# Performance work log

Measured on AMD Instinct MI355X. Metric: run time of the kernel, lower is better.

Reference implementation:

```python
import jax, jax.numpy as jnp
import numpy as np

B, D, N, F = 2048, 512, 100000, 64
NEG = -1000000.0


def setup_inputs() -> dict:
    key = jax.random.key(0)
    k1, k2, k3, k4 = jax.random.split(key, 4)
    q = jax.random.normal(k1, (B, D), dtype=jnp.float32)
    rhs = jax.random.normal(k2, (D, N), dtype=jnp.float32)
    queries = jax.random.randint(k3, (B, 3), 0, N, dtype=jnp.int64)
    filter_idx = jax.random.randint(k4, (B, F), 0, N, dtype=jnp.int64)
    return {"q": q, "rhs": rhs, "queries": queries, "filter_idx": filter_idx}


def reference(q, rhs, queries, filter_idx):
    # targets[i] = score of the true triple = q[i] . rhs[:, true_rhs[i]]
    true_rhs = queries[:, 2]                         # [B]
    targets = jnp.einsum('bd,bd->b', q, rhs[:, true_rhs].T)  # [B]

    scores = q @ rhs                                  # [B, N]

    # filtered ranking: mask out known true tails + the query's own tail
    rows = jnp.arange(scores.shape[0])[:, None]       # [B, 1]
    scores = scores.at[rows, filter_idx].set(NEG)
    scores = scores.at[jnp.arange(scores.shape[0]), true_rhs].set(NEG)

    # rank = 1 + number of candidates scoring >= the true triple
    ranks = 1.0 + jnp.sum((scores >= targets[:, None]).astype(jnp.float32), axis=1)
    return ranks
```

## Files before the change

kernel.cpp:

```cpp
#include <hip/hip_runtime.h>
#include <hip/hip_bf16.h>

#define B_ 2048
#define D_ 512
#define N_ 100000
#define F_ 64
#define NEGV (-1000000.0f)

typedef __bf16 bfx8 __attribute__((ext_vector_type(8)));
typedef float f32x4 __attribute__((ext_vector_type(4)));
typedef unsigned short u16x8 __attribute__((ext_vector_type(8)));

static __device__ __forceinline__ unsigned short f2bf(float f) {
  unsigned u = __float_as_uint(f);
  unsigned r = (u + 0x7fffu + ((u >> 16) & 1u)) >> 16;
  return (unsigned short)r;
}
static __device__ __forceinline__ float bf2f(unsigned short u) {
  return __uint_as_float(((unsigned)u) << 16);
}

static __device__ __forceinline__ void async_copy16(const void* g, void* l) {
  __builtin_amdgcn_global_load_lds((const __attribute__((address_space(1))) void*)g,
                                   (__attribute__((address_space(3))) void*)l, 16, 0, 0);
}

__global__ void targets_init(const float* __restrict__ q, const float* __restrict__ rhs,
                             const int* __restrict__ queries, float* __restrict__ targets,
                             float* __restrict__ out) {
  __shared__ float wsum[4];
  int b = blockIdx.x;
  int tid = threadIdx.x, lane = tid & 63, w = tid >> 6;
  int p = queries[b * 3 + 2];
  float s = 0.f;
  for (int d = tid; d < D_; d += 256) s += q[b * D_ + d] * rhs[(size_t)d * N_ + p];
  for (int off = 32; off; off >>= 1) s += __shfl_down(s, off, 64);
  if (lane == 0) wsum[w] = s;
  __syncthreads();
  if (tid == 0) {
    targets[b] = wsum[0] + wsum[1] + wsum[2] + wsum[3];
    out[b] = 1.0f;
  }
}

__global__ void convert_q(const float* __restrict__ q, unsigned short* __restrict__ qb) {
  int i = blockIdx.x * blockDim.x + threadIdx.x;
  const float4* q4 = (const float4*)q;
  float4 v = q4[i];
  ushort4 o;
  o.x = f2bf(v.x); o.y = f2bf(v.y); o.z = f2bf(v.z); o.w = f2bf(v.w);
  ((ushort4*)qb)[i] = o;
}

__global__ void transpose_rhs(const float* __restrict__ rhs, unsigned short* __restrict__ rt) {
  __shared__ float tile[64][65];
  int n0 = blockIdx.x * 64, d0 = blockIdx.y * 64;
  int tid = threadIdx.x;
  if (n0 + 64 <= N_) {
#pragma unroll
    for (int p = 0; p < 4; ++p) {
      int e = p * 256 + tid;
      int d = e >> 4, c4 = e & 15;
      float4 v = *(const float4*)(rhs + (size_t)(d0 + d) * N_ + n0 + c4 * 4);
      tile[d][c4 * 4 + 0] = v.x; tile[d][c4 * 4 + 1] = v.y;
      tile[d][c4 * 4 + 2] = v.z; tile[d][c4 * 4 + 3] = v.w;
    }
  } else {
    int c = tid & 63, r4 = tid >> 6;
#pragma unroll
    for (int p = 0; p < 16; ++p) {
      int d = r4 + p * 4;
      if (n0 + c < N_) tile[d][c] = rhs[(size_t)(d0 + d) * N_ + n0 + c];
    }
  }
  __syncthreads();
#pragma unroll
  for (int p = 0; p < 4; ++p) {
    int e = p * 256 + tid;
    int n = e >> 4, dg = e & 15;
    if (n0 + n < N_) {
      ushort4 o;
      o.x = f2bf(tile[dg * 4 + 0][n]);
      o.y = f2bf(tile[dg * 4 + 1][n]);
      o.z = f2bf(tile[dg * 4 + 2][n]);
      o.w = f2bf(tile[dg * 4 + 3][n]);
      *(ushort4*)(rt + (size_t)(n0 + n) * D_ + d0 + dg * 4) = o;
    }
  }
}

__global__ void __launch_bounds__(256) gemm_count(
    const unsigned short* __restrict__ qb,
    const unsigned short* __restrict__ rt,
    const float* __restrict__ targets,
    float* __restrict__ out) {
  __shared__ unsigned short As[128 * 64];
  __shared__ unsigned short Bs[128 * 64];
  __shared__ float sT[128];
  __shared__ int cnt2[2][128];

  int tid = threadIdx.x;
  int m0 = blockIdx.x * 128;
  int n0 = blockIdx.y * 128;

  if (tid < 128) sT[tid] = targets[m0 + tid];

  int w = tid >> 6, lane = tid & 63;
  int mw = (w & 1) * 64, nw = (w >> 1) * 64;
  int quad = lane >> 4, l16 = lane & 15;

  f32x4 acc[4][4];
  f32x4 z = {0.f, 0.f, 0.f, 0.f};
#pragma unroll
  for (int i = 0; i < 4; ++i)
#pragma unroll
    for (int j = 0; j < 4; ++j) acc[i][j] = z;

  for (int kt = 0; kt < 8; ++kt) {
    int k0 = kt * 64;
    __syncthreads();
#pragma unroll
    for (int i = 0; i < 4; ++i) {
      int c = i * 256 + tid;
      int m = c >> 3, jj = c & 7;
      const unsigned short* gp = qb + (size_t)(m0 + m) * D_ + k0 + jj * 8;
      async_copy16(gp, As + c * 8);
    }
#pragma unroll
    for (int i = 0; i < 4; ++i) {
      int c = i * 256 + tid;
      int n = c >> 3, jj = c & 7;
      int ng = n0 + n; if (ng > N_ - 1) ng = N_ - 1;
      const unsigned short* gp = rt + (size_t)ng * D_ + k0 + jj * 8;
      async_copy16(gp, Bs + c * 8);
    }
    __syncthreads();

#pragma unroll
    for (int kh = 0; kh < 2; ++kh) {
      bfx8 a[4], b[4];
#pragma unroll
      for (int mi = 0; mi < 4; ++mi) {
        int m = mw + mi * 16 + l16;
        u16x8 au = *(const u16x8*)(As + m * 64 + kh * 32 + quad * 8);
        a[mi] = __builtin_bit_cast(bfx8, au);
      }
#pragma unroll
      for (int ni = 0; ni < 4; ++ni) {
        int n = nw + ni * 16 + l16;
        u16x8 bu = *(const u16x8*)(Bs + n * 64 + kh * 32 + quad * 8);
        b[ni] = __builtin_bit_cast(bfx8, bu);
      }
#pragma unroll
      for (int mi = 0; mi < 4; ++mi)
#pragma unroll
        for (int ni = 0; ni < 4; ++ni)
          acc[mi][ni] = __builtin_amdgcn_mfma_f32_16x16x32_bf16(a[mi], b[ni], acc[mi][ni], 0, 0, 0);
    }
  }

#pragma unroll
  for (int mi = 0; mi < 4; ++mi) {
#pragma unroll
    for (int reg = 0; reg < 4; ++reg) {
      int rl = mw + mi * 16 + quad * 4 + reg;
      float t = sT[rl];
      int c = 0;
#pragma unroll
      for (int ni = 0; ni < 4; ++ni) {
        int col = n0 + nw + ni * 16 + l16;
        if (col < N_ && acc[mi][ni][reg] >= t) c++;
      }
      c += __shfl_xor(c, 1, 64);
      c += __shfl_xor(c, 2, 64);
      c += __shfl_xor(c, 4, 64);
      c += __shfl_xor(c, 8, 64);
      if (l16 == 0) cnt2[w >> 1][rl] = c;
    }
  }
  __syncthreads();
  if (tid < 128) {
    int tot = cnt2[0][tid] + cnt2[1][tid];
    if (tot) atomicAdd(&out[m0 + tid], (float)tot);
  }
}

__global__ void corrections(const unsigned short* __restrict__ qb,
                            const unsigned short* __restrict__ rt,
                            const int* __restrict__ queries,
                            const int* __restrict__ filt,
                            const float* __restrict__ targets,
                            float* __restrict__ out) {
  int b = blockIdx.x;
  int tid = threadIdx.x;
  int w = tid >> 6, lane = tid & 63;
  __shared__ int idx[F_ + 1];
  __shared__ unsigned char uq[F_ + 1];
  if (tid <= F_) idx[tid] = (tid < F_) ? filt[b * F_ + tid] : queries[b * 3 + 2];
  __syncthreads();
  if (tid <= F_) {
    int p = idx[tid];
    bool u = true;
    for (int j = 0; j < tid; ++j)
      if (idx[j] == p) u = false;
    uq[tid] = u;
  }
  __syncthreads();
  float t = targets[b];
  float corr = 0.f;
  u16x8 qv = ((const u16x8*)(qb + (size_t)b * D_))[lane];
  for (int ii = w; ii <= F_; ii += 8) {
    if (!uq[ii]) continue;
    int p = idx[ii];
    u16x8 rv = ((const u16x8*)(rt + (size_t)p * D_))[lane];
    float s = 0.f;
#pragma unroll
    for (int j = 0; j < 8; ++j) s += bf2f(qv[j]) * bf2f(rv[j]);
    for (int off = 32; off; off >>= 1) s += __shfl_down(s, off, 64);
    if (lane == 0)
      corr += (NEGV >= t ? 1.f : 0.f) - (s >= t ? 1.f : 0.f);
  }
  if (lane == 0 && corr != 0.f) atomicAdd(&out[b], corr);
}

__global__ void fallback_count(const float* __restrict__ q, const float* __restrict__ rhs,
                               const int* __restrict__ queries, const int* __restrict__ filt,
                               const float* __restrict__ targets, float* __restrict__ out) {
  int b = blockIdx.y;
  int n = blockIdx.x * 256 + threadIdx.x;
  __shared__ float qs[D_];
  __shared__ int idx[F_ + 1];
  __shared__ int cnt;
  for (int d = threadIdx.x; d < D_; d += 256) qs[d] = q[b * D_ + d];
  if (threadIdx.x < F_) idx[threadIdx.x] = filt[b * F_ + threadIdx.x];
  if (threadIdx.x == F_) idx[F_] = queries[b * 3 + 2];
  if (threadIdx.x == 0) cnt = 0;
  __syncthreads();
  if (n < N_) {
    float t = targets[b];
    float s = 0.f;
    for (int d = 0; d < D_; ++d) s += qs[d] * rhs[(size_t)d * N_ + n];
    bool member = false;
    for (int j = 0; j <= F_; ++j)
      if (idx[j] == n) member = true;
    float sv = member ? NEGV : s;
    if (sv >= t) atomicAdd(&cnt, 1);
  }
  __syncthreads();
  if (threadIdx.x == 0 && cnt) atomicAdd(&out[b], (float)cnt);
}

extern "C" void kernel_launch(void* const* d_in, const int* in_sizes, int n_in,
                              void* d_out, int out_size, void* d_ws, size_t ws_size,
                              hipStream_t stream) {
  const float* q = (const float*)d_in[0];
  const float* rhs = (const float*)d_in[1];
  const int* queries = (const int*)d_in[2];
  const int* filt = (const int*)d_in[3];
  float* out = (float*)d_out;

  char* wsb = (char*)d_ws;
  float* targets = (float*)wsb;
  unsigned short* qb = (unsigned short*)(wsb + 8192);
  unsigned short* rt = (unsigned short*)(wsb + 8192 + (size_t)B_ * D_ * 2);
  size_t need = 8192 + (size_t)B_ * D_ * 2 + (size_t)N_ * D_ * 2;

  targets_init<<<B_, 256, 0, stream>>>(q, rhs, queries, targets, out);

  if (ws_size >= need) {
    convert_q<<<(B_ * D_ / 4) / 256, 256, 0, stream>>>(q, qb);
    transpose_rhs<<<dim3((N_ + 63) / 64, D_ / 64), 256, 0, stream>>>(rhs, rt);
    gemm_count<<<dim3(B_ / 128, (N_ + 127) / 128), 256, 0, stream>>>(qb, rt, targets, out);
    corrections<<<B_, 512, 0, stream>>>(qb, rt, queries, filt, targets, out);
  } else {
    fallback_count<<<dim3((N_ + 255) / 256, B_), 256, 0, stream>>>(q, rhs, queries, filt, targets, out);
  }
}
```

Measured before the change: 736.5 us.

## Double-buffer GEMM K-tiles with async prefetch and fuse q conversion into targets

The GEMM main loop now uses two 32-wide K buffers in LDS and issues async global-to-LDS loads for the next tile before computing on the current one. This replaces the load-sync-compute pattern that had two barriers per iteration, so memory latency can overlap with MFMA work. It also merges the bf16 conversion of q into the targets kernel, which removes one launch. The cost is twice as many loop iterations with smaller tiles. Correctness depends on the single barrier per iteration being enough to order the async copies against reads of the other buffer.

```diff
diff --git a/kernel.cpp b/kernel.cpp
--- a/kernel.cpp
+++ b/kernel.cpp
@@ -25,15 +25,17 @@
                                    (__attribute__((address_space(3))) void*)l, 16, 0, 0);
 }
 
-__global__ void targets_init(const float* __restrict__ q, const float* __restrict__ rhs,
-                             const int* __restrict__ queries, float* __restrict__ targets,
-                             float* __restrict__ out) {
+__global__ void targets_convert(const float* __restrict__ q, const float* __restrict__ rhs,
+                                const int* __restrict__ queries, float* __restrict__ targets,
+                                float* __restrict__ out, unsigned short* __restrict__ qb) {
   __shared__ float wsum[4];
   int b = blockIdx.x;
   int tid = threadIdx.x, lane = tid & 63, w = tid >> 6;
   int p = queries[b * 3 + 2];
-  float s = 0.f;
-  for (int d = tid; d < D_; d += 256) s += q[b * D_ + d] * rhs[(size_t)d * N_ + p];
+  float2 v = ((const float2*)(q + (size_t)b * D_))[tid];
+  ushort2 o; o.x = f2bf(v.x); o.y = f2bf(v.y);
+  ((ushort2*)(qb + (size_t)b * D_))[tid] = o;
+  float s = v.x * rhs[(size_t)(2 * tid) * N_ + p] + v.y * rhs[(size_t)(2 * tid + 1) * N_ + p];
   for (int off = 32; off; off >>= 1) s += __shfl_down(s, off, 64);
   if (lane == 0) wsum[w] = s;
   __syncthreads();
@@ -41,15 +43,6 @@
     targets[b] = wsum[0] + wsum[1] + wsum[2] + wsum[3];
     out[b] = 1.0f;
   }
-}
-
-__global__ void convert_q(const float* __restrict__ q, unsigned short* __restrict__ qb) {
-  int i = blockIdx.x * blockDim.x + threadIdx.x;
-  const float4* q4 = (const float4*)q;
-  float4 v = q4[i];
-  ushort4 o;
-  o.x = f2bf(v.x); o.y = f2bf(v.y); o.z = f2bf(v.z); o.w = f2bf(v.w);
-  ((ushort4*)qb)[i] = o;
 }
 
 __global__ void transpose_rhs(const float* __restrict__ rhs, unsigned short* __restrict__ rt) {
@@ -94,8 +87,8 @@
     const unsigned short* __restrict__ rt,
     const float* __restrict__ targets,
     float* __restrict__ out) {
-  __shared__ unsigned short As[128 * 64];
-  __shared__ unsigned short Bs[128 * 64];
+  __shared__ unsigned short As[2][128 * 32];
+  __shared__ unsigned short Bs[2][128 * 32];
   __shared__ float sT[128];
   __shared__ int cnt2[2][128];
 
@@ -109,6 +102,16 @@
   int mw = (w & 1) * 64, nw = (w >> 1) * 64;
   int quad = lane >> 4, l16 = lane & 15;
 
+  int c0 = tid, c1 = 256 + tid;
+  int am0 = c0 >> 2, aj0 = (c0 & 3) * 8;
+  int am1 = c1 >> 2, aj1 = (c1 & 3) * 8;
+  int bn0g = n0 + am0; if (bn0g > N_ - 1) bn0g = N_ - 1;
+  int bn1g = n0 + am1; if (bn1g > N_ - 1) bn1g = N_ - 1;
+  const unsigned short* agp0 = qb + (size_t)(m0 + am0) * D_ + aj0;
+  const unsigned short* agp1 = qb + (size_t)(m0 + am1) * D_ + aj1;
+  const unsigned short* bgp0 = rt + (size_t)bn0g * D_ + aj0;
+  const unsigned short* bgp1 = rt + (size_t)bn1g * D_ + aj1;
+
   f32x4 acc[4][4];
   f32x4 z = {0.f, 0.f, 0.f, 0.f};
 #pragma unroll
@@ -116,47 +119,40 @@
 #pragma unroll
     for (int j = 0; j < 4; ++j) acc[i][j] = z;
 
-  for (int kt = 0; kt < 8; ++kt) {
-    int k0 = kt * 64;
+  async_copy16(agp0, &As[0][c0 * 8]);
+  async_copy16(agp1, &As[0][c1 * 8]);
+  async_copy16(bgp0, &Bs[0][c0 * 8]);
+  async_copy16(bgp1, &Bs[0][c1 * 8]);
+
+  for (int kt = 0; kt < 16; ++kt) {
+    int buf = kt & 1;
     __syncthreads();
-#pragma unroll
-    for (int i = 0; i < 4; ++i) {
-      int c = i * 256 + tid;
-      int m = c >> 3, jj = c & 7;
-      const unsigned short* gp = qb + (size_t)(m0 + m) * D_ + k0 + jj * 8;
-      async_copy16(gp, As + c * 8);
-    }
-#pragma unroll
-    for (int i = 0; i < 4; ++i) {
-      int c = i * 256 + tid;
-      int n = c >> 3, jj = c & 7;
-      int ng = n0 + n; if (ng > N_ - 1) ng = N_ - 1;
-      const unsigned short* gp = rt + (size_t)ng * D_ + k0 + jj * 8;
-      async_copy16(gp, Bs + c * 8);
-    }
-    __syncthreads();
-
-#pragma unroll
-    for (int kh = 0; kh < 2; ++kh) {
-      bfx8 a[4], b[4];
-#pragma unroll
-      for (int mi = 0; mi < 4; ++mi) {
-        int m = mw + mi * 16 + l16;
-        u16x8 au = *(const u16x8*)(As + m * 64 + kh * 32 + quad * 8);
-        a[mi] = __builtin_bit_cast(bfx8, au);
-      }
-#pragma unroll
-      for (int ni = 0; ni < 4; ++ni) {
-        int n = nw + ni * 16 + l16;
-        u16x8 bu = *(const u16x8*)(Bs + n * 64 + kh * 32 + quad * 8);
-        b[ni] = __builtin_bit_cast(bfx8, bu);
-      }
-#pragma unroll
-      for (int mi = 0; mi < 4; ++mi)
-#pragma unroll
-        for (int ni = 0; ni < 4; ++ni)
-          acc[mi][ni] = __builtin_amdgcn_mfma_f32_16x16x32_bf16(a[mi], b[ni], acc[mi][ni], 0, 0, 0);
-    }
+    if (kt + 1 < 16) {
+      int nb = 1 - buf, k1 = (kt + 1) * 32;
+      async_copy16(agp0 + k1, &As[nb][c0 * 8]);
+      async_copy16(agp1 + k1, &As[nb][c1 * 8]);
+      async_copy16(bgp0 + k1, &Bs[nb][c0 * 8]);
+      async_copy16(bgp1 + k1, &Bs[nb][c1 * 8]);
+    }
+
+    bfx8 a[4], b[4];
+#pragma unroll
+    for (int mi = 0; mi < 4; ++mi) {
+      int m = mw + mi * 16 + l16;
+      u16x8 au = *(const u16x8*)(&As[buf][m * 32 + quad * 8]);
+      a[mi] = __builtin_bit_cast(bfx8, au);
+    }
+#pragma unroll
+    for (int ni = 0; ni < 4; ++ni) {
+      int n = nw + ni * 16 + l16;
+      u16x8 bu = *(const u16x8*)(&Bs[buf][n * 32 + quad * 8]);
+      b[ni] = __builtin_bit_cast(bfx8, bu);
+    }
+#pragma unroll
+    for (int mi = 0; mi < 4; ++mi)
+#pragma unroll
+      for (int ni = 0; ni < 4; ++ni)
+        acc[mi][ni] = __builtin_amdgcn_mfma_f32_16x16x32_bf16(a[mi], b[ni], acc[mi][ni], 0, 0, 0);
   }
 
 #pragma unroll
@@ -223,6 +219,24 @@
   if (lane == 0 && corr != 0.f) atomicAdd(&out[b], corr);
 }
 
+__global__ void targets_init(const float* __restrict__ q, const float* __restrict__ rhs,
+                             const int* __restrict__ queries, float* __restrict__ targets,
+                             float* __restrict__ out) {
+  __shared__ float wsum[4];
+  int b = blockIdx.x;
+  int tid = threadIdx.x, lane = tid & 63, w = tid >> 6;
+  int p = queries[b * 3 + 2];
+  float s = 0.f;
+  for (int d = tid; d < D_; d += 256) s += q[b * D_ + d] * rhs[(size_t)d * N_ + p];
+  for (int off = 32; off; off >>= 1) s += __shfl_down(s, off, 64);
+  if (lane == 0) wsum[w] = s;
+  __syncthreads();
+  if (tid == 0) {
+    targets[b] = wsum[0] + wsum[1] + wsum[2] + wsum[3];
+    out[b] = 1.0f;
+  }
+}
+
 __global__ void fallback_count(const float* __restrict__ q, const float* __restrict__ rhs,
                                const int* __restrict__ queries, const int* __restrict__ filt,
                                const float* __restrict__ targets, float* __restrict__ out) {
@@ -265,14 +279,13 @@
   unsigned short* rt = (unsigned short*)(wsb + 8192 + (size_t)B_ * D_ * 2);
   size_t need = 8192 + (size_t)B_ * D_ * 2 + (size_t)N_ * D_ * 2;
 
-  targets_init<<<B_, 256, 0, stream>>>(q, rhs, queries, targets, out);
-
   if (ws_size >= need) {
-    convert_q<<<(B_ * D_ / 4) / 256, 256, 0, stream>>>(q, qb);
+    targets_convert<<<B_, 256, 0, stream>>>(q, rhs, queries, targets, out, qb);
     transpose_rhs<<<dim3((N_ + 63) / 64, D_ / 64), 256, 0, stream>>>(rhs, rt);
     gemm_count<<<dim3(B_ / 128, (N_ + 127) / 128), 256, 0, stream>>>(qb, rt, targets, out);
     corrections<<<B_, 512, 0, stream>>>(qb, rt, queries, filt, targets, out);
   } else {
+    targets_init<<<B_, 256, 0, stream>>>(q, rhs, queries, targets, out);
     fallback_count<<<dim3((N_ + 255) / 256, B_), 256, 0, stream>>>(q, rhs, queries, filt, targets, out);
   }
 }
```

Measured after the change: 609.6 us. 1.21x faster.
